# Kernel tuning notes

Hardware: AMD Instinct MI355X
Metric: run time of the kernel (lower is better)

Reference implementation:

```python
import jax, jax.numpy as jnp
import numpy as np

N = 32768   # 'a' nodes
K = 8       # incoming edges per node (regular graph)
K2 = K // 2
E = N * K   # edges, stored as reverse pairs (2i, 2i+1)
D = 300     # hid_dim
H = 4       # attention heads
DEPTH = 3


def _build_graph():
    i = np.arange(N)
    src = np.empty(E, np.int64)
    mail = np.empty((N, K), np.int64)
    for d in range(1, K2 + 1):
        base = 2 * (i * K2 + (d - 1))
        src[base] = i                 # edge i -> (i+d)%N
        src[base + 1] = (i + d) % N   # reverse edge (i+d)%N -> i
        # incoming edges of node v: ((v-d)->v) and ((v+d)->v)
        mail[:, 2 * (d - 1)] = 2 * (((i - d) % N) * K2 + (d - 1))
        mail[:, 2 * (d - 1) + 1] = 2 * (i * K2 + (d - 1)) + 1
    return src, mail


def setup_inputs() -> dict:
    key = jax.random.key(0)
    ks = jax.random.split(key, 12)
    s = 1.0 / np.sqrt(D)
    src, mail = _build_graph()
    return {
        'f': jax.random.normal(ks[0], (N, D), jnp.float32),
        'x': jax.random.normal(ks[1], (E, D), jnp.float32),
        'mail_idx': jnp.asarray(mail),
        'src_idx': jnp.asarray(src),
        'Wq': jax.random.normal(ks[2], (D, D), jnp.float32) * s,
        'bq': jnp.zeros((D,), jnp.float32),
        'Wk': jax.random.normal(ks[3], (D, D), jnp.float32) * s,
        'bk': jnp.zeros((D,), jnp.float32),
        'Wv': jax.random.normal(ks[4], (D, D), jnp.float32) * s,
        'bv': jnp.zeros((D,), jnp.float32),
        'Wo': jax.random.normal(ks[5], (D, D), jnp.float32) * s,
        'bo': jnp.zeros((D,), jnp.float32),
        'Wmp': jax.random.normal(ks[6], (DEPTH - 1, D, D), jnp.float32) * s,
        'bmp': jnp.zeros((DEPTH - 1, D), jnp.float32),
        'Wlast': jax.random.normal(ks[7], (3 * D, D), jnp.float32) * s,
        'blast': jnp.zeros((D,), jnp.float32),
    }


def _mha(q_in, k_in, v_in, Wq, bq, Wk, bk, Wv, bv, Wo, bo):
    # q_in: [N,1,D], k_in/v_in: [N,K,D]  (per-node neighborhood attention)
    dk = D // H
    q = (q_in @ Wq + bq).reshape(N, 1, H, dk).transpose(0, 2, 1, 3)
    k = (k_in @ Wk + bk).reshape(N, -1, H, dk).transpose(0, 2, 1, 3)
    v = (v_in @ Wv + bv).reshape(N, -1, H, dk).transpose(0, 2, 1, 3)
    scores = jnp.einsum('nhqd,nhkd->nhqk', q, k) / jnp.sqrt(jnp.float32(dk))
    p = jax.nn.softmax(scores, axis=-1)
    o = jnp.einsum('nhqk,nhkd->nhqd', p, v).transpose(0, 2, 1, 3).reshape(N, 1, D)
    return o @ Wo + bo


def reference(f, x, mail_idx, src_idx, Wq, bq, Wk, bk, Wv, bv, Wo, bo,
              Wmp, bmp, Wlast, blast):
    rev = jnp.arange(E) ^ 1  # reverse_edge: swap within consecutive pairs
    f_h = f              # init_node: f_h = f.clone()
    h = x                # init_edge: h = x.clone()
    for i in range(DEPTH - 1):
        mail = h[mail_idx]                    # copy_e mailbox [N,K,D]
        feat = f_h[:, None, :]                # [N,1,D]
        # add_attn: attn(feat, mail, mail + feat)
        f_h = _mha(feat, mail, mail + feat,
                   Wq, bq, Wk, bk, Wv, bv, Wo, bo)[:, 0, :]
        rev_h = h[rev]                        # paired reverse-edge feature
        m = f_h[src_idx] - rev_h              # del_reverse_message
        h = jax.nn.relu(x + m @ Wmp[i] + bmp[i])  # update_edge
    # final node update: Linear(cat([sum(mailbox h), f_h, f]))
    mail_sum = jnp.sum(h[mail_idx], axis=1)   # [N,D]
    f_final = jnp.concatenate([mail_sum, f_h, f], axis=1) @ Wlast + blast
    return f_final
```

## Files before the change

kernel.cpp:

```cpp
#include <hip/hip_runtime.h>

typedef unsigned short u16;
typedef unsigned int u32;
typedef __bf16 bf16x8 __attribute__((ext_vector_type(8)));
typedef float f32x4 __attribute__((ext_vector_type(4)));

#define N_NODES 32768
#define E_EDGES 262144
#define BQ_U16 26240
#define S75 0.11547005383792515f

__device__ __forceinline__ float b2f(u16 u) {
    union { u32 u; float f; } x; x.u = ((u32)u) << 16; return x.f;
}
__device__ __forceinline__ u16 f2b(float f) {
    union { float f; u32 u; } x; x.f = f;
    u32 r = x.u + 0x7FFF + ((x.u >> 16) & 1);
    return (u16)(r >> 16);
}

#define GLOAD16(g, l) \
    __builtin_amdgcn_global_load_lds((const __attribute__((address_space(1))) u32*)(g), \
                                     (__attribute__((address_space(3))) u32*)(l), 16, 0, 0)

__global__ void convT_k(const float* __restrict__ src, int R, int C,
                        u16* __restrict__ dst, int KP_, long total) {
    long id = (long)blockIdx.x * blockDim.x + threadIdx.x;
    if (id >= total) return;
    int n = (int)(id / KP_), k = (int)(id % KP_);
    dst[id] = (k < R && n < C) ? f2b(src[(long)k * C + n]) : (u16)0;
}

__global__ void convTq_k(const float* __restrict__ src, u16* __restrict__ dst) {
    int id = blockIdx.x * 256 + threadIdx.x;
    if (id >= 4 * BQ_U16) return;
    int q = id / BQ_U16, rem = id % BQ_U16;
    int r = rem / 328, c = rem % 328;
    int n = q * 80 + r;
    dst[id] = (c < 300 && n < 300) ? f2b(src[(long)c * 300 + n]) : (u16)0;
}

__global__ void wqkq_k(const float* __restrict__ Wq, const float* __restrict__ Wk,
                       u16* __restrict__ dst) {
    int id = blockIdx.x * 256 + threadIdx.x;
    if (id >= 16 * BQ_U16) return;
    int q = id / BQ_U16, rem = id % BQ_U16;
    int r = rem / 328, c = rem % 328;
    int h = q >> 2;
    int cc = (q & 3) * 80 + r;
    float acc = 0.f;
    if (c < 300 && cc < 300) {
        const float* wq = Wq + (long)c * 300 + 75 * h;
        const float* wk = Wk + (long)cc * 300 + 75 * h;
        for (int d = 0; d < 75; ++d) acc += wq[d] * wk[d];
        acc *= S75;
    }
    dst[id] = f2b(acc);
}

__global__ void bqk_k(const float* __restrict__ bq, const float* __restrict__ Wk,
                      float* __restrict__ dst) {
    int n = blockIdx.x * 256 + threadIdx.x;
    if (n >= 1280) return;
    int h = n / 320, cc = n % 320;
    float acc = 0.f;
    if (cc < 300) {
        const float* b = bq + 75 * h;
        const float* wk = Wk + (long)cc * 300 + 75 * h;
        for (int d = 0; d < 75; ++d) acc += b[d] * wk[d];
        acc *= S75;
    }
    dst[n] = acc;
}

__global__ void ucatp_k(const float* __restrict__ Wv, const float* __restrict__ Wo,
                        u16* __restrict__ dst) {
    long id = (long)blockIdx.x * 256 + threadIdx.x;
    if (id >= 4L * 5 * BQ_U16) return;
    int q = (int)(id / (5 * BQ_U16));
    int rem = (int)(id % (5 * BQ_U16));
    int ph = rem / BQ_U16;
    int rem2 = rem % BQ_U16;
    int r = rem2 / 328, c = rem2 % 328;
    int n = q * 80 + r;
    float acc = 0.f;
    if (n < 300 && c < 320) {
        if (ph < 4) {
            int a = c;
            if (a < 300) {
                const float* wv = Wv + (long)a * 300 + 75 * ph;
                const float* wo = Wo + (long)(75 * ph) * 300 + n;
                for (int d = 0; d < 75; ++d) acc += wv[d] * wo[(long)d * 300];
            }
        } else {
            int a = c;
            if (a < 300) {
                const float* wv = Wv + (long)a * 300;
                const float* wo = Wo + n;
                for (int d = 0; d < 300; ++d) acc += wv[d] * wo[(long)d * 300];
            }
        }
    }
    dst[id] = f2b(acc);
}

__global__ void bvo_k(const float* __restrict__ bv, const float* __restrict__ Wo,
                      const float* __restrict__ bo, float* __restrict__ dst) {
    int n = blockIdx.x * 256 + threadIdx.x;
    if (n >= 320) return;
    float acc = 0.f;
    if (n < 300) {
        for (int d = 0; d < 300; ++d) acc += bv[d] * Wo[(long)d * 300 + n];
        acc += bo[n];
    }
    dst[n] = acc;
}

__global__ void padconv_k(const float* __restrict__ src, int C,
                          u16* __restrict__ dst, int CP,
                          u16* __restrict__ dst2, int CP2, long total) {
    long id = (long)blockIdx.x * blockDim.x + threadIdx.x;
    if (id >= total) return;
    int cw = CP >> 3;
    long row = id / cw;
    int c8 = (int)(id % cw) * 8;
    u32 w[4];
    #pragma unroll
    for (int p = 0; p < 4; ++p) {
        int c0 = c8 + 2 * p, c1 = c0 + 1;
        u16 lo = (c0 < C) ? f2b(src[row * C + c0]) : (u16)0;
        u16 hi = (c1 < C) ? f2b(src[row * C + c1]) : (u16)0;
        w[p] = (u32)lo | ((u32)hi << 16);
    }
    u32* d = (u32*)(dst + row * CP + c8);
    d[0] = w[0]; d[1] = w[1]; d[2] = w[2]; d[3] = w[3];
    if (dst2) {
        u32* d2 = (u32*)(dst2 + row * CP2 + c8);
        d2[0] = w[0]; d2[1] = w[1]; d2[2] = w[2]; d2[3] = w[3];
    }
}

__global__ void featcopy_k(const u16* __restrict__ src, u16* __restrict__ dst) {
    long id = (long)blockIdx.x * 256 + threadIdx.x;
    if (id >= (long)N_NODES * 40) return;
    long row = id / 40;
    int c8 = (int)(id % 40) * 8;
    *(uint4*)&dst[row * 1600 + 1280 + c8] = *(const uint4*)&src[row * 320 + c8];
}

#define TCOMP(KB, APTR) do { \
    bf16x8 av_[2], bb_[5]; \
    _Pragma("unroll") for (int fr = 0; fr < 2; ++fr) \
        av_[fr] = *(const bf16x8*)&(APTR)[ar0 + fr * 512]; \
    _Pragma("unroll") for (int fc = 0; fc < 5; ++fc) \
        bb_[fc] = *(const bf16x8*)&Bs[br0 + fc * 5248 + (KB) * 32]; \
    __builtin_amdgcn_s_setprio(1); \
    _Pragma("unroll") for (int fr = 0; fr < 2; ++fr) \
        _Pragma("unroll") for (int fc = 0; fc < 5; ++fc) \
            acc[fr][fc] = __builtin_amdgcn_mfma_f32_16x16x32_bf16(bb_[fc], av_[fr], acc[fr][fc], 0, 0, 0); \
    __builtin_amdgcn_s_setprio(0); \
} while (0)

template<int QBITS, int OSTR>
__global__ __launch_bounds__(256, 2) void ngemm_k(
    const u16* __restrict__ A, const u16* __restrict__ Bswz,
    const float* __restrict__ bias, u16* __restrict__ outB)
{
    __shared__ __attribute__((aligned(16))) u16 Bs[80 * 328];
    __shared__ __attribute__((aligned(16))) u16 As3[3][128 * 32];
    const int tid = threadIdx.x;
    const int wf = tid >> 6, lane = tid & 63;
    const int tl = lane & 15, thi = lane >> 4;
    const int bid = blockIdx.x;
    const int gid = (bid & 7) * ((int)gridDim.x >> 3) + (bid >> 3);
    const long m0 = (long)(gid >> QBITS) * 128;
    const int q = gid & ((1 << QBITS) - 1);
    const int n0 = q * 80;
    const int wf_u = __builtin_amdgcn_readfirstlane(wf);
    const u16* Bsrc = Bswz + q * BQ_U16;

    #pragma unroll
    for (int i = 0; i < 13; ++i) {
        int t = i * 256 + tid;
        if (t < 3280)
            GLOAD16(Bsrc + (long)t * 8, &Bs[(i * 256 + wf_u * 64) * 8]);
    }
    const int r1 = tid >> 2;
    const int g1 = (tid & 3) ^ ((r1 >> 1) & 3);
    const u16* gA0 = A + (m0 + r1) * 320L + g1 * 8;
    const u16* gA1 = A + (m0 + 64 + r1) * 320L + g1 * 8;

#define ESTAGE(KB) { \
    GLOAD16(gA0 + (KB) * 32, &As3[(KB) % 3][wf_u * 512]); \
    GLOAD16(gA1 + (KB) * 32, &As3[(KB) % 3][2048 + wf_u * 512]); }

    ESTAGE(0); ESTAGE(1);

    f32x4 acc[2][5];
    #pragma unroll
    for (int i = 0; i < 2; ++i)
        #pragma unroll
        for (int j = 0; j < 5; ++j) acc[i][j] = (f32x4)(0.f);
    const int ar0 = (wf * 32 + tl) * 32 + (thi ^ ((tl >> 1) & 3)) * 8;
    const int br0 = tl * 328 + thi * 8;

#define ESTEP(KB, VN) { \
    asm volatile("s_waitcnt vmcnt(" #VN ")" ::: "memory"); \
    __builtin_amdgcn_s_barrier(); \
    __builtin_amdgcn_sched_barrier(0); \
    if ((KB) + 2 < 10) ESTAGE((KB) + 2); \
    TCOMP(KB, (&As3[(KB) % 3][0])); }

    ESTEP(0, 2) ESTEP(1, 2) ESTEP(2, 2) ESTEP(3, 2) ESTEP(4, 2)
    ESTEP(5, 2) ESTEP(6, 2) ESTEP(7, 2) ESTEP(8, 2) ESTEP(9, 0)
#undef ESTEP
#undef ESTAGE

    #pragma unroll
    for (int fr = 0; fr < 2; ++fr) {
        const long row = m0 + wf * 32 + fr * 16 + tl;
        #pragma unroll
        for (int fc = 0; fc < 5; ++fc) {
            const int c0 = n0 + fc * 16 + thi * 4;
            f32x4 v = acc[fr][fc];
            if (bias) {
                const float4 bs = *(const float4*)&bias[c0];
                v[0] += bs.x; v[1] += bs.y; v[2] += bs.z; v[3] += bs.w;
            }
            uint2 p;
            p.x = (u32)f2b(v[0]) | ((u32)f2b(v[1]) << 16);
            p.y = (u32)f2b(v[2]) | ((u32)f2b(v[3]) << 16);
            *(uint2*)&outB[row * (long)OSTR + c0] = p;
        }
    }
}

__global__ __launch_bounds__(256, 2) void hgemm_k(
    const u16* __restrict__ A , const u16* __restrict__ Bswz ,
    const u16* __restrict__ FG, const u16* __restrict__ hx,
    const int* __restrict__ srcidx, const float* __restrict__ bias,
    u16* __restrict__ outB)
{
    __shared__ __attribute__((aligned(16))) u16 Bs[80 * 328];
    __shared__ __attribute__((aligned(16))) u16 As3[3][128 * 32];
    const int tid = threadIdx.x;
    const int wf = tid >> 6, lane = tid & 63;
    const int tl = lane & 15, thi = lane >> 4;
    const int bid = blockIdx.x;
    const int gid = (bid & 7) * ((int)gridDim.x >> 3) + (bid >> 3);
    const long m0 = (long)(gid >> 2) * 128;
    const int q = gid & 3;
    const int n0 = q * 80;
    const int wf_u = __builtin_amdgcn_readfirstlane(wf);
    const u16* Bsrc = Bswz + q * BQ_U16;

    #pragma unroll
    for (int i = 0; i < 13; ++i) {
        int t = i * 256 + tid;
        if (t < 3280)
            GLOAD16(Bsrc + (long)t * 8, &Bs[(i * 256 + wf_u * 64) * 8]);
    }
    const int r1 = tid >> 2;
    const int g1 = (tid & 3) ^ ((r1 >> 1) & 3);
    const u16* gA0 = A + (m0 + r1) * 320L + g1 * 8;
    const u16* gA1 = A + (m0 + 64 + r1) * 320L + g1 * 8;

#define HSTAGE(KB) { \
    GLOAD16(gA0 + (KB) * 32, &As3[(KB) % 3][wf_u * 512]); \
    GLOAD16(gA1 + (KB) * 32, &As3[(KB) % 3][2048 + wf_u * 512]); }

    HSTAGE(0); HSTAGE(1);

    f32x4 acc[2][5];
    #pragma unroll
    for (int i = 0; i < 2; ++i)
        #pragma unroll
        for (int j = 0; j < 5; ++j) acc[i][j] = (f32x4)(0.f);
    const int ar0 = (wf * 32 + tl) * 32 + (thi ^ ((tl >> 1) & 3)) * 8;
    const int br0 = tl * 328 + thi * 8;

#define HSTEP(KB, VN) { \
    asm volatile("s_waitcnt vmcnt(" #VN ")" ::: "memory"); \
    __builtin_amdgcn_s_barrier(); \
    __builtin_amdgcn_sched_barrier(0); \
    if ((KB) + 2 < 10) HSTAGE((KB) + 2); \
    TCOMP(KB, (&As3[(KB) % 3][0])); }

    HSTEP(0, 2) HSTEP(1, 2) HSTEP(2, 2) HSTEP(3, 2) HSTEP(4, 2)
    HSTEP(5, 2) HSTEP(6, 2) HSTEP(7, 2) HSTEP(8, 2) HSTEP(9, 0)
#undef HSTEP
#undef HSTAGE

    #pragma unroll
    for (int fr = 0; fr < 2; ++fr) {
        const long row = m0 + wf * 32 + fr * 16 + tl;
        const int srow = srcidx[row];
        #pragma unroll
        for (int fc = 0; fc < 5; ++fc) {
            const int c0 = n0 + fc * 16 + thi * 4;
            float o0 = __shfl_xor(acc[fr][fc][0], 1, 64);
            float o1 = __shfl_xor(acc[fr][fc][1], 1, 64);
            float o2 = __shfl_xor(acc[fr][fc][2], 1, 64);
            float o3 = __shfl_xor(acc[fr][fc][3], 1, 64);
            const ushort4 fg = *(const ushort4*)&FG[(long)srow * 320 + c0];
            const ushort4 xv = *(const ushort4*)&hx[row * 320 + c0];
            float v0 = b2f(fg.x) + b2f(xv.x) - o0;
            float v1 = b2f(fg.y) + b2f(xv.y) - o1;
            float v2 = b2f(fg.z) + b2f(xv.z) - o2;
            float v3 = b2f(fg.w) + b2f(xv.w) - o3;
            if (c0 < 300) {
                const float4 bs = *(const float4*)&bias[c0];
                v0 += bs.x; v1 += bs.y; v2 += bs.z; v3 += bs.w;
            }
            v0 = fmaxf(v0, 0.f); v1 = fmaxf(v1, 0.f);
            v2 = fmaxf(v2, 0.f); v3 = fmaxf(v3, 0.f);
            uint2 p;
            p.x = (u32)f2b(v0) | ((u32)f2b(v1) << 16);
            p.y = (u32)f2b(v2) | ((u32)f2b(v3) << 16);
            *(uint2*)&outB[row * 320 + c0] = p;
        }
    }
}

__global__ __launch_bounds__(256, 2) void wgemm_k(
    const u16* __restrict__ A , const u16* __restrict__ Bp ,
    const float* __restrict__ bias , u16* __restrict__ outB )
{
    __shared__ __attribute__((aligned(16))) u16 Bs[80 * 328];
    __shared__ __attribute__((aligned(16))) u16 As3[3][128 * 32];
    const int tid = threadIdx.x;
    const int wf = tid >> 6, lane = tid & 63;
    const int tl = lane & 15, thi = lane >> 4;
    const int bid = blockIdx.x;
    const int gid = (bid & 7) * ((int)gridDim.x >> 3) + (bid >> 3);
    const long m0 = (long)(gid >> 2) * 128;
    const int q = gid & 3;
    const int n0 = q * 80;
    const int wf_u = __builtin_amdgcn_readfirstlane(wf);
    const u16* BsrcQ = Bp + (long)q * (5 * BQ_U16);

    const int r1 = tid >> 2;
    const int g1 = (tid & 3) ^ ((r1 >> 1) & 3);
    const u16* gA0 = A + (m0 + r1) * 1600L + g1 * 8;
    const u16* gA1 = A + (m0 + 64 + r1) * 1600L + g1 * 8;

    f32x4 acc[2][5];
    #pragma unroll
    for (int i = 0; i < 2; ++i)
        #pragma unroll
        for (int j = 0; j < 5; ++j) acc[i][j] = (f32x4)(0.f);
    const int ar0 = (wf * 32 + tl) * 32 + (thi ^ ((tl >> 1) & 3)) * 8;
    const int br0 = tl * 328 + thi * 8;

    #pragma unroll
    for (int ph = 0; ph < 5; ++ph) {
        if (ph) __syncthreads();
        const u16* Bsrc = BsrcQ + ph * BQ_U16;
        #pragma unroll
        for (int i = 0; i < 13; ++i) {
            int t = i * 256 + tid;
            if (t < 3280)
                GLOAD16(Bsrc + (long)t * 8, &Bs[(i * 256 + wf_u * 64) * 8]);
        }
        const long ko = (long)ph * 320;

#define WSTAGE(KB) { \
    GLOAD16(gA0 + ko + (KB) * 32, &As3[(KB) % 3][wf_u * 512]); \
    GLOAD16(gA1 + ko + (KB) * 32, &As3[(KB) % 3][2048 + wf_u * 512]); }

        WSTAGE(0); WSTAGE(1);

#define WSTEP(KB, VN) { \
    asm volatile("s_waitcnt vmcnt(" #VN ")" ::: "memory"); \
    __builtin_amdgcn_s_barrier(); \
    __builtin_amdgcn_sched_barrier(0); \
    if ((KB) + 2 < 10) WSTAGE((KB) + 2); \
    TCOMP(KB, (&As3[(KB) % 3][0])); }

        WSTEP(0, 2) WSTEP(1, 2) WSTEP(2, 2) WSTEP(3, 2) WSTEP(4, 2)
        WSTEP(5, 2) WSTEP(6, 2) WSTEP(7, 2) WSTEP(8, 2) WSTEP(9, 0)
#undef WSTEP
#undef WSTAGE
    }

    #pragma unroll
    for (int fr = 0; fr < 2; ++fr) {
        const long row = m0 + wf * 32 + fr * 16 + tl;
        #pragma unroll
        for (int fc = 0; fc < 5; ++fc) {
            const int c0 = n0 + fc * 16 + thi * 4;
            f32x4 v = acc[fr][fc];
            const float4 bs = *(const float4*)&bias[c0];
            v[0] += bs.x; v[1] += bs.y; v[2] += bs.z; v[3] += bs.w;
            uint2 p;
            p.x = (u32)f2b(v[0]) | ((u32)f2b(v[1]) << 16);
            p.y = (u32)f2b(v[2]) | ((u32)f2b(v[3]) << 16);
            *(uint2*)&outB[row * 320 + c0] = p;
        }
    }
}

__global__ __launch_bounds__(256) void attn2_k(
    const u16* __restrict__ qg, const u16* __restrict__ hcur,
    const int* __restrict__ mail, u16* __restrict__ wideA)
{
    const int tid = threadIdx.x;
    const long n = (long)blockIdx.x * 4 + (tid >> 6);
    const int lane = tid & 63;
    const bool act = lane < 40;
    const int ll = act ? lane : 39;

    int idx[8];
    #pragma unroll
    for (int j = 0; j < 8; ++j) idx[j] = mail[n * 8 + j];
    uint4 hr[8];
    #pragma unroll
    for (int j = 0; j < 8; ++j)
        hr[j] = *(const uint4*)&hcur[(long)idx[j] * 320 + ll * 8];
    uint4 qv[4];
    #pragma unroll
    for (int h = 0; h < 4; ++h)
        qv[h] = *(const uint4*)&qg[n * 1280 + h * 320 + ll * 8];
    if (!act) {
        #pragma unroll
        for (int j = 0; j < 8; ++j) hr[j] = make_uint4(0, 0, 0, 0);
    }

    float qf[4][8];
    #pragma unroll
    for (int h = 0; h < 4; ++h) {
        const u32 w[4] = {qv[h].x, qv[h].y, qv[h].z, qv[h].w};
        #pragma unroll
        for (int p = 0; p < 4; ++p) {
            qf[h][2 * p]     = b2f((u16)(w[p] & 0xFFFF));
            qf[h][2 * p + 1] = b2f((u16)(w[p] >> 16));
        }
    }

    float s[4][8];
    #pragma unroll
    for (int j = 0; j < 8; ++j) {
        float hf[8];
        const u32 w[4] = {hr[j].x, hr[j].y, hr[j].z, hr[j].w};
        #pragma unroll
        for (int p = 0; p < 4; ++p) {
            hf[2 * p]     = b2f((u16)(w[p] & 0xFFFF));
            hf[2 * p + 1] = b2f((u16)(w[p] >> 16));
        }
        #pragma unroll
        for (int h = 0; h < 4; ++h) {
            float d = 0.f;
            #pragma unroll
            for (int m = 0; m < 8; ++m) d += qf[h][m] * hf[m];
            d += __shfl_xor(d, 32, 64);
            d += __shfl_xor(d, 16, 64);
            d += __shfl_xor(d, 8, 64);
            d += __shfl_xor(d, 4, 64);
            d += __shfl_xor(d, 2, 64);
            d += __shfl_xor(d, 1, 64);
            s[h][j] = d;
        }
    }

    float p_[4][8];
    #pragma unroll
    for (int h = 0; h < 4; ++h) {
        float mx = s[h][0];
        #pragma unroll
        for (int j = 1; j < 8; ++j) mx = fmaxf(mx, s[h][j]);
        float sum = 0.f;
        #pragma unroll
        for (int j = 0; j < 8; ++j) { p_[h][j] = __expf(s[h][j] - mx); sum += p_[h][j]; }
        const float inv = 1.f / sum;
        #pragma unroll
        for (int j = 0; j < 8; ++j) p_[h][j] *= inv;
    }

    float y[4][8];
    #pragma unroll
    for (int h = 0; h < 4; ++h)
        #pragma unroll
        for (int m = 0; m < 8; ++m) y[h][m] = 0.f;
    #pragma unroll
    for (int j = 0; j < 8; ++j) {
        float hf[8];
        const u32 w[4] = {hr[j].x, hr[j].y, hr[j].z, hr[j].w};
        #pragma unroll
        for (int p = 0; p < 4; ++p) {
            hf[2 * p]     = b2f((u16)(w[p] & 0xFFFF));
            hf[2 * p + 1] = b2f((u16)(w[p] >> 16));
        }
        #pragma unroll
        for (int h = 0; h < 4; ++h)
            #pragma unroll
            for (int m = 0; m < 8; ++m) y[h][m] += p_[h][j] * hf[m];
    }
    if (act) {
        #pragma unroll
        for (int h = 0; h < 4; ++h) {
            uint4 o;
            o.x = (u32)f2b(y[h][0]) | ((u32)f2b(y[h][1]) << 16);
            o.y = (u32)f2b(y[h][2]) | ((u32)f2b(y[h][3]) << 16);
            o.z = (u32)f2b(y[h][4]) | ((u32)f2b(y[h][5]) << 16);
            o.w = (u32)f2b(y[h][6]) | ((u32)f2b(y[h][7]) << 16);
            *(uint4*)&wideA[n * 1600 + h * 320 + lane * 8] = o;
        }
    }
}

#define LOADB(bq, kt1) { const long ko_ = (long)(kt1) << 6; \
    _Pragma("unroll") for (int fc = 0; fc < 5; ++fc) \
      _Pragma("unroll") for (int ks = 0; ks < 2; ++ks) \
        bq[fc][ks] = *(const bf16x8*)(gBw + (long)fc * 16 * KP + ko_ + ks * 32); }

#define READA(lkt) { \
    _Pragma("unroll") for (int fr = 0; fr < 4; ++fr) \
      _Pragma("unroll") for (int ks = 0; ks < 2; ++ks) \
        a[fr][ks] = *(const bf16x8*)&As[(fr * 16 + tl) * 320 + ((((lkt) * 8 + ks * 4 + thi) ^ sx) * 8)]; }

#define DOMFMA(bq) { _Pragma("unroll") for (int fr = 0; fr < 4; ++fr) \
    _Pragma("unroll") for (int fc = 0; fc < 5; ++fc) \
      _Pragma("unroll") for (int ks = 0; ks < 2; ++ks) \
        acc[fr][fc] = __builtin_amdgcn_mfma_f32_16x16x32_bf16(bq[fc][ks], a[fr][ks], acc[fr][fc], 0, 0, 0); }

template<int KP>
__global__ __launch_bounds__(256, 2) void gemm_k(
    const u16* __restrict__ A,
    const u16* __restrict__ BT,
    const float* __restrict__ bias,
    float* __restrict__ outF, int ostride, int ocols)
{
    __shared__ u16 As[64 * 320];
    const int tid = threadIdx.x;
    const int w = tid >> 6, lane = tid & 63;
    const int tl = lane & 15, thi = lane >> 4;
    const int sx = tl & 7;
    const long m0 = (long)blockIdx.x * 64;
    const int w_u = __builtin_amdgcn_readfirstlane(w);

    const u16* gBw = BT + ((long)(w * 80 + tl)) * KP + thi * 8;

    f32x4 acc[4][5];
    #pragma unroll
    for (int i = 0; i < 4; ++i)
        #pragma unroll
        for (int j = 0; j < 5; ++j) acc[i][j] = (f32x4)(0.f);

    constexpr int NCH = KP / 320;
    constexpr int NST = KP >> 6;
    bf16x8 bA[5][2], bB[5][2], a[4][2];

    #pragma unroll
    for (int kb = 0; kb < NCH; ++kb) {
        if (kb) __syncthreads();
        #pragma unroll
        for (int i = 0; i < 10; ++i) {
            const int c = i * 256 + w_u * 64 + lane;
            const int r = c / 40, s = c - r * 40;
            GLOAD16(A + (m0 + r) * (long)KP + kb * 320 + ((s ^ (r & 7)) * 8),
                    &As[(i * 256 + w_u * 64) * 8]);
        }
        if (kb == 0) LOADB(bA, 0);
        __syncthreads();
        #pragma unroll
        for (int lkt = 0; lkt < 5; ++lkt) {
            const int kt = kb * 5 + lkt;
            if (kt + 1 < NST) {
                if (kt & 1) { LOADB(bA, kt + 1); } else { LOADB(bB, kt + 1); }
            }
            READA(lkt);
            if (kt & 1) { DOMFMA(bB); } else { DOMFMA(bA); }
        }
    }

    #pragma unroll
    for (int fr = 0; fr < 4; ++fr) {
        const long row = m0 + fr * 16 + tl;
        #pragma unroll
        for (int fc = 0; fc < 5; ++fc) {
            const int c0 = w * 80 + fc * 16 + thi * 4;
            f32x4 v = acc[fr][fc];
            if (bias && c0 < 300) {
                const float4 bs = *(const float4*)&bias[c0];
                v[0] += bs.x; v[1] += bs.y; v[2] += bs.z; v[3] += bs.w;
            }
            if (c0 < ocols)
                *(float4*)&outF[row * (long)ostride + c0] = make_float4(v[0], v[1], v[2], v[3]);
        }
    }
}

__global__ __launch_bounds__(256) void concat_k(
    const u16* __restrict__ hb, const u16* __restrict__ fhb,
    const float* __restrict__ f, const int* __restrict__ mail,
    u16* __restrict__ Acat)
{
    const long n = blockIdx.x;
    int m[8];
    #pragma unroll
    for (int j = 0; j < 8; ++j) m[j] = mail[n * 8 + j];
    for (int c = threadIdx.x; c < 960; c += 256) {
        float v;
        if (c < 300) {
            float s = 0.f;
            #pragma unroll
            for (int j = 0; j < 8; ++j) s += b2f(hb[(long)m[j] * 320 + c]);
            v = s;
        } else if (c < 600) v = b2f(fhb[n * 320 + (c - 300)]);
        else if (c < 900) v = f[n * 300 + (c - 600)];
        else v = 0.f;
        Acat[n * 960 + c] = f2b(v);
    }
}

extern "C" void kernel_launch(void* const* d_in, const int* in_sizes, int n_in,
                              void* d_out, int out_size, void* d_ws, size_t ws_size,
                              hipStream_t stream)
{
    const int N = N_NODES, E = E_EDGES;
    const float* f    = (const float*)d_in[0];
    const float* x    = (const float*)d_in[1];
    const int*   mail = (const int*)d_in[2];
    const int*   srcx = (const int*)d_in[3];
    const float* Wq = (const float*)d_in[4];   const float* bq = (const float*)d_in[5];
    const float* Wk = (const float*)d_in[6];
    const float* Wv = (const float*)d_in[8];   const float* bv = (const float*)d_in[9];
    const float* Wo = (const float*)d_in[10];  const float* bo = (const float*)d_in[11];
    const float* Wmp = (const float*)d_in[12]; const float* bmp = (const float*)d_in[13];
    const float* Wlast = (const float*)d_in[14]; const float* blast = (const float*)d_in[15];
    float* out = (float*)d_out;

    char* ws = (char*)d_ws;
    size_t off = 0;
    auto alloc = [&](size_t b) -> void* {
        void* p = ws + off; off += (b + 255) & ~(size_t)255; return p;
    };
    u16* hb    = (u16*)alloc((size_t)E * 320 * 2);
    u16* hb2   = (u16*)alloc((size_t)E * 320 * 2);
    u16* qgb   = (u16*)alloc((size_t)N * 1280 * 2);
    u16* wideA = (u16*)alloc((size_t)N * 1600 * 2);
    u16* fhb   = (u16*)alloc((size_t)N * 320 * 2);
    u16* FGb   = (u16*)alloc((size_t)N * 320 * 2);
    u16* Acat  = (u16*)alloc((size_t)N * 960 * 2);
    u16* WqkS  = (u16*)alloc((size_t)16 * BQ_U16 * 2);
    u16* Wm0S  = (u16*)alloc((size_t)4 * BQ_U16 * 2);
    u16* Wm1S  = (u16*)alloc((size_t)4 * BQ_U16 * 2);
    u16* UcatP = (u16*)alloc((size_t)4 * 5 * BQ_U16 * 2);
    u16* WcatB = (u16*)alloc((size_t)960 * 320 * 2);
    float* bqkF = (float*)alloc(1280 * 4);
    float* bvoF = (float*)alloc(320 * 4);

    {
        wqkq_k<<<(16 * BQ_U16 + 255) / 256, 256, 0, stream>>>(Wq, Wk, WqkS);
        bqk_k<<<5, 256, 0, stream>>>(bq, Wk, bqkF);
        ucatp_k<<<(int)((4L * 5 * BQ_U16 + 255) / 256), 256, 0, stream>>>(Wv, Wo, UcatP);
        bvo_k<<<2, 256, 0, stream>>>(bv, Wo, bo, bvoF);
        int blks = (4 * BQ_U16 + 255) / 256;
        convTq_k<<<blks, 256, 0, stream>>>(Wmp, Wm0S);
        convTq_k<<<blks, 256, 0, stream>>>(Wmp + 90000, Wm1S);
        long totc = (long)320 * 960;
        convT_k<<<(int)((totc + 255) / 256), 256, 0, stream>>>(Wlast, 900, 300, WcatB, 960, totc);
    }
    {
        long totE = (long)E * 40;
        padconv_k<<<(int)((totE + 255) / 256), 256, 0, stream>>>(x, 300, hb, 320, nullptr, 0, totE);
        long totN = (long)N * 40;
        padconv_k<<<(int)((totN + 255) / 256), 256, 0, stream>>>(f, 300, fhb, 320, wideA + 1280, 1600, totN);
    }

    const int GQG = (N / 128) * 16;
    const int GNQ = (N / 128) * 4;
    const int GEH = (E / 128) * 4;

    for (int it = 0; it < 2; ++it) {
        const float* bmpi = bmp + it * 300;
        const u16* WmS = it ? Wm1S : Wm0S;
        const u16* hcur = it ? hb2 : hb;
        u16* hnxt = it ? hb : hb2;
        ngemm_k<4, 1280><<<GQG, 256, 0, stream>>>(fhb, WqkS, bqkF, qgb);
        attn2_k<<<N / 4, 256, 0, stream>>>(qgb, hcur, mail, wideA);
        wgemm_k<<<GNQ, 256, 0, stream>>>(wideA, UcatP, bvoF, fhb);
        featcopy_k<<<(int)(((long)N * 40 + 255) / 256), 256, 0, stream>>>(fhb, wideA);
        ngemm_k<2, 320><<<GNQ, 256, 0, stream>>>(fhb, WmS, nullptr, FGb);
        hgemm_k<<<GEH, 256, 0, stream>>>(hcur, WmS, FGb, hb, srcx, bmpi, hnxt);
    }

    concat_k<<<N, 256, 0, stream>>>(hb, fhb, f, mail, Acat);
    gemm_k<960><<<N / 64, 256, 0, stream>>>(Acat, WcatB, blast, out, 300, 300);
}
```

Before: 1.395 ms.

## Use 1024-thread 512-row tiles for node and edge GEMMs to amortize B loads

The ngemm and hgemm kernels move from 256-thread blocks with 128-row M tiles to 1024-thread blocks with 512-row tiles. Each wavefront now owns its own 32-row A slab, staged three K-blocks deep. The shared 80-column B panel is loaded once per block, so its global traffic and LDS fill are spread over four times as many rows. Per-K-step block barriers are replaced by per-wave vmcnt/lgkmcnt waits, because each wave only reads A data it loaded itself. In exchange, grids get smaller, the block needs more LDS and must fit 16 waves, and a few lanes issue dummy B loads into a scratch buffer.

```diff
diff --git a/kernel.cpp b/kernel.cpp
--- a/kernel.cpp
+++ b/kernel.cpp
@@ -148,77 +148,91 @@
     *(uint4*)&dst[row * 1600 + 1280 + c8] = *(const uint4*)&src[row * 320 + c8];
 }
 
-#define TCOMP(KB, APTR) do { \
-    bf16x8 av_[2], bb_[5]; \
-    _Pragma("unroll") for (int fr = 0; fr < 2; ++fr) \
-        av_[fr] = *(const bf16x8*)&(APTR)[ar0 + fr * 512]; \
-    _Pragma("unroll") for (int fc = 0; fc < 5; ++fc) \
-        bb_[fc] = *(const bf16x8*)&Bs[br0 + fc * 5248 + (KB) * 32]; \
+
+#define GEMM16_SHARED \
+    __shared__ __attribute__((aligned(16))) u16 Bs[3328 * 8];      \
+    __shared__ __attribute__((aligned(16))) u16 dumpB[512];        \
+    __shared__ __attribute__((aligned(16))) u16 As3[3][512 * 32];
+
+#define GEMM16_PRE(QBITS, LDA) \
+    const int tid = threadIdx.x; \
+    const int w = tid >> 6, lane = tid & 63; \
+    const int tl = lane & 15, thi = lane >> 4; \
+    const int bid = blockIdx.x; \
+    const int gid = (bid & 7) * ((int)gridDim.x >> 3) + (bid >> 3); \
+    const long m0 = (long)(gid >> (QBITS)) * 512; \
+    const int q = gid & ((1 << (QBITS)) - 1); \
+    const int n0 = q * 80; \
+    const int w_u = __builtin_amdgcn_readfirstlane(w); \
+    const u16* Bsrc = Bswz + q * BQ_U16; \
+     \
+    _Pragma("unroll") \
+    for (int i = 0; i < 3; ++i) \
+        GLOAD16(Bsrc + (long)(i * 1024 + tid) * 8, &Bs[(i * 1024 + w_u * 64) * 8]); \
+    { \
+        int t = 3072 + tid; \
+        int ts = t < 3280 ? t : 3279; \
+        u16* bdst = (w_u < 4) ? &Bs[(3072 + w_u * 64) * 8] : dumpB; \
+        GLOAD16(Bsrc + (long)ts * 8, bdst); \
+    } \
+    __builtin_amdgcn_sched_barrier(0); \
+     \
+    const int rr = lane >> 2;                  \
+    const int gsrc = (lane & 3) ^ (rr & 3);    \
+    const u16* pA0 = A + (m0 + w * 32 + rr) * (long)(LDA) + gsrc * 8; \
+    const u16* pA1 = pA0 + 16L * (LDA); \
+    u16* awbase = &As3[0][0];
+
+#define ASTAGE16(KB) { \
+    u16* d_ = &As3[(KB) % 3][w_u * 1024]; \
+    GLOAD16(pA0 + (KB) * 32, d_); \
+    GLOAD16(pA1 + (KB) * 32, d_ + 512); }
+
+#define TCOMP16(KB) { \
+    const u16* aw_ = &As3[(KB) % 3][w * 1024]; \
+    bf16x8 a0_ = *(const bf16x8*)&aw_[tl * 32 + (thi ^ (tl & 3)) * 8]; \
+    bf16x8 a1_ = *(const bf16x8*)&aw_[512 + tl * 32 + (thi ^ (tl & 3)) * 8]; \
     __builtin_amdgcn_s_setprio(1); \
-    _Pragma("unroll") for (int fr = 0; fr < 2; ++fr) \
-        _Pragma("unroll") for (int fc = 0; fc < 5; ++fc) \
-            acc[fr][fc] = __builtin_amdgcn_mfma_f32_16x16x32_bf16(bb_[fc], av_[fr], acc[fr][fc], 0, 0, 0); \
-    __builtin_amdgcn_s_setprio(0); \
-} while (0)
+    _Pragma("unroll") for (int fc = 0; fc < 5; ++fc) { \
+        bf16x8 bb_ = *(const bf16x8*)&Bs[tl * 328 + thi * 8 + fc * 5248 + (KB) * 32]; \
+        acc[0][fc] = __builtin_amdgcn_mfma_f32_16x16x32_bf16(bb_, a0_, acc[0][fc], 0, 0, 0); \
+        acc[1][fc] = __builtin_amdgcn_mfma_f32_16x16x32_bf16(bb_, a1_, acc[1][fc], 0, 0, 0); } \
+    __builtin_amdgcn_s_setprio(0); }
+
+#define GEMM16_LOOP \
+    ASTAGE16(0); ASTAGE16(1); ASTAGE16(2); \
+    f32x4 acc[2][5]; \
+    _Pragma("unroll") for (int i = 0; i < 2; ++i) \
+        _Pragma("unroll") for (int j = 0; j < 5; ++j) acc[i][j] = (f32x4)(0.f); \
+    asm volatile("s_waitcnt vmcnt(6)" ::: "memory");    \
+    __builtin_amdgcn_s_barrier();                       \
+    __builtin_amdgcn_sched_barrier(0); \
+     \
+    _Pragma("unroll") \
+    for (int KB = 0; KB < 10; ++KB) { \
+        if (KB <= 7)      { asm volatile("s_waitcnt vmcnt(4)" ::: "memory"); } \
+        else if (KB == 8) { asm volatile("s_waitcnt vmcnt(2)" ::: "memory"); } \
+        else              { asm volatile("s_waitcnt vmcnt(0)" ::: "memory"); } \
+        __builtin_amdgcn_sched_barrier(0); \
+        TCOMP16(KB); \
+        asm volatile("s_waitcnt lgkmcnt(0)" ::: "memory");   \
+        __builtin_amdgcn_sched_barrier(0); \
+        if (KB + 3 < 10) ASTAGE16(KB + 3); \
+    } \
+    (void)awbase;
 
 template<int QBITS, int OSTR>
-__global__ __launch_bounds__(256, 2) void ngemm_k(
+__global__ __launch_bounds__(1024, 4) void ngemm16_k(
     const u16* __restrict__ A, const u16* __restrict__ Bswz,
     const float* __restrict__ bias, u16* __restrict__ outB)
 {
-    __shared__ __attribute__((aligned(16))) u16 Bs[80 * 328];
-    __shared__ __attribute__((aligned(16))) u16 As3[3][128 * 32];
-    const int tid = threadIdx.x;
-    const int wf = tid >> 6, lane = tid & 63;
-    const int tl = lane & 15, thi = lane >> 4;
-    const int bid = blockIdx.x;
-    const int gid = (bid & 7) * ((int)gridDim.x >> 3) + (bid >> 3);
-    const long m0 = (long)(gid >> QBITS) * 128;
-    const int q = gid & ((1 << QBITS) - 1);
-    const int n0 = q * 80;
-    const int wf_u = __builtin_amdgcn_readfirstlane(wf);
-    const u16* Bsrc = Bswz + q * BQ_U16;
-
-    #pragma unroll
-    for (int i = 0; i < 13; ++i) {
-        int t = i * 256 + tid;
-        if (t < 3280)
-            GLOAD16(Bsrc + (long)t * 8, &Bs[(i * 256 + wf_u * 64) * 8]);
-    }
-    const int r1 = tid >> 2;
-    const int g1 = (tid & 3) ^ ((r1 >> 1) & 3);
-    const u16* gA0 = A + (m0 + r1) * 320L + g1 * 8;
-    const u16* gA1 = A + (m0 + 64 + r1) * 320L + g1 * 8;
-
-#define ESTAGE(KB) { \
-    GLOAD16(gA0 + (KB) * 32, &As3[(KB) % 3][wf_u * 512]); \
-    GLOAD16(gA1 + (KB) * 32, &As3[(KB) % 3][2048 + wf_u * 512]); }
-
-    ESTAGE(0); ESTAGE(1);
-
-    f32x4 acc[2][5];
-    #pragma unroll
-    for (int i = 0; i < 2; ++i)
-        #pragma unroll
-        for (int j = 0; j < 5; ++j) acc[i][j] = (f32x4)(0.f);
-    const int ar0 = (wf * 32 + tl) * 32 + (thi ^ ((tl >> 1) & 3)) * 8;
-    const int br0 = tl * 328 + thi * 8;
-
-#define ESTEP(KB, VN) { \
-    asm volatile("s_waitcnt vmcnt(" #VN ")" ::: "memory"); \
-    __builtin_amdgcn_s_barrier(); \
-    __builtin_amdgcn_sched_barrier(0); \
-    if ((KB) + 2 < 10) ESTAGE((KB) + 2); \
-    TCOMP(KB, (&As3[(KB) % 3][0])); }
-
-    ESTEP(0, 2) ESTEP(1, 2) ESTEP(2, 2) ESTEP(3, 2) ESTEP(4, 2)
-    ESTEP(5, 2) ESTEP(6, 2) ESTEP(7, 2) ESTEP(8, 2) ESTEP(9, 0)
-#undef ESTEP
-#undef ESTAGE
+    GEMM16_SHARED
+    GEMM16_PRE(QBITS, 320)
+    GEMM16_LOOP
 
     #pragma unroll
     for (int fr = 0; fr < 2; ++fr) {
-        const long row = m0 + wf * 32 + fr * 16 + tl;
+        const long row = m0 + w * 32 + fr * 16 + tl;
         #pragma unroll
         for (int fc = 0; fc < 5; ++fc) {
             const int c0 = n0 + fc * 16 + thi * 4;
@@ -235,65 +249,19 @@
     }
 }
 
-__global__ __launch_bounds__(256, 2) void hgemm_k(
+__global__ __launch_bounds__(1024, 4) void hgemm16_k(
     const u16* __restrict__ A , const u16* __restrict__ Bswz ,
     const u16* __restrict__ FG, const u16* __restrict__ hx,
     const int* __restrict__ srcidx, const float* __restrict__ bias,
     u16* __restrict__ outB)
 {
-    __shared__ __attribute__((aligned(16))) u16 Bs[80 * 328];
-    __shared__ __attribute__((aligned(16))) u16 As3[3][128 * 32];
-    const int tid = threadIdx.x;
-    const int wf = tid >> 6, lane = tid & 63;
-    const int tl = lane & 15, thi = lane >> 4;
-    const int bid = blockIdx.x;
-    const int gid = (bid & 7) * ((int)gridDim.x >> 3) + (bid >> 3);
-    const long m0 = (long)(gid >> 2) * 128;
-    const int q = gid & 3;
-    const int n0 = q * 80;
-    const int wf_u = __builtin_amdgcn_readfirstlane(wf);
-    const u16* Bsrc = Bswz + q * BQ_U16;
-
-    #pragma unroll
-    for (int i = 0; i < 13; ++i) {
-        int t = i * 256 + tid;
-        if (t < 3280)
-            GLOAD16(Bsrc + (long)t * 8, &Bs[(i * 256 + wf_u * 64) * 8]);
-    }
-    const int r1 = tid >> 2;
-    const int g1 = (tid & 3) ^ ((r1 >> 1) & 3);
-    const u16* gA0 = A + (m0 + r1) * 320L + g1 * 8;
-    const u16* gA1 = A + (m0 + 64 + r1) * 320L + g1 * 8;
-
-#define HSTAGE(KB) { \
-    GLOAD16(gA0 + (KB) * 32, &As3[(KB) % 3][wf_u * 512]); \
-    GLOAD16(gA1 + (KB) * 32, &As3[(KB) % 3][2048 + wf_u * 512]); }
-
-    HSTAGE(0); HSTAGE(1);
-
-    f32x4 acc[2][5];
-    #pragma unroll
-    for (int i = 0; i < 2; ++i)
-        #pragma unroll
-        for (int j = 0; j < 5; ++j) acc[i][j] = (f32x4)(0.f);
-    const int ar0 = (wf * 32 + tl) * 32 + (thi ^ ((tl >> 1) & 3)) * 8;
-    const int br0 = tl * 328 + thi * 8;
-
-#define HSTEP(KB, VN) { \
-    asm volatile("s_waitcnt vmcnt(" #VN ")" ::: "memory"); \
-    __builtin_amdgcn_s_barrier(); \
-    __builtin_amdgcn_sched_barrier(0); \
-    if ((KB) + 2 < 10) HSTAGE((KB) + 2); \
-    TCOMP(KB, (&As3[(KB) % 3][0])); }
-
-    HSTEP(0, 2) HSTEP(1, 2) HSTEP(2, 2) HSTEP(3, 2) HSTEP(4, 2)
-    HSTEP(5, 2) HSTEP(6, 2) HSTEP(7, 2) HSTEP(8, 2) HSTEP(9, 0)
-#undef HSTEP
-#undef HSTAGE
+    GEMM16_SHARED
+    GEMM16_PRE(2, 320)
+    GEMM16_LOOP
 
     #pragma unroll
     for (int fr = 0; fr < 2; ++fr) {
-        const long row = m0 + wf * 32 + fr * 16 + tl;
+        const long row = m0 + w * 32 + fr * 16 + tl;
         const int srow = srcidx[row];
         #pragma unroll
         for (int fc = 0; fc < 5; ++fc) {
@@ -322,11 +290,24 @@
     }
 }
 
+#define TCOMP(KB, APTR) do { \
+    bf16x8 av_[2], bb_[5]; \
+    _Pragma("unroll") for (int fr = 0; fr < 2; ++fr) \
+        av_[fr] = *(const bf16x8*)&(APTR)[ar0 + fr * 512]; \
+    _Pragma("unroll") for (int fc = 0; fc < 5; ++fc) \
+        bb_[fc] = *(const bf16x8*)&Bsw[br0 + fc * 5248 + (KB) * 32]; \
+    __builtin_amdgcn_s_setprio(1); \
+    _Pragma("unroll") for (int fr = 0; fr < 2; ++fr) \
+        _Pragma("unroll") for (int fc = 0; fc < 5; ++fc) \
+            acc[fr][fc] = __builtin_amdgcn_mfma_f32_16x16x32_bf16(bb_[fc], av_[fr], acc[fr][fc], 0, 0, 0); \
+    __builtin_amdgcn_s_setprio(0); \
+} while (0)
+
 __global__ __launch_bounds__(256, 2) void wgemm_k(
-    const u16* __restrict__ A , const u16* __restrict__ Bp ,
-    const float* __restrict__ bias , u16* __restrict__ outB )
+    const u16* __restrict__ A , const u16* __restrict__ Bp,
+    const float* __restrict__ bias, u16* __restrict__ outB)
 {
-    __shared__ __attribute__((aligned(16))) u16 Bs[80 * 328];
+    __shared__ __attribute__((aligned(16))) u16 Bsw[80 * 328];
     __shared__ __attribute__((aligned(16))) u16 As3[3][128 * 32];
     const int tid = threadIdx.x;
     const int wf = tid >> 6, lane = tid & 63;
@@ -360,7 +341,7 @@
         for (int i = 0; i < 13; ++i) {
             int t = i * 256 + tid;
             if (t < 3280)
-                GLOAD16(Bsrc + (long)t * 8, &Bs[(i * 256 + wf_u * 64) * 8]);
+                GLOAD16(Bsrc + (long)t * 8, &Bsw[(i * 256 + wf_u * 64) * 8]);
         }
         const long ko = (long)ph * 320;
 
@@ -668,21 +649,22 @@
         padconv_k<<<(int)((totN + 255) / 256), 256, 0, stream>>>(f, 300, fhb, 320, wideA + 1280, 1600, totN);
     }
 
-    const int GQG = (N / 128) * 16;
-    const int GNQ = (N / 128) * 4;
-    const int GEH = (E / 128) * 4;
+    const int GQG = (N / 512) * 16;
+    const int GFG = (N / 512) * 4;
+    const int GNW = (N / 128) * 4;
+    const int GEH = (E / 512) * 4;
 
     for (int it = 0; it < 2; ++it) {
         const float* bmpi = bmp + it * 300;
         const u16* WmS = it ? Wm1S : Wm0S;
         const u16* hcur = it ? hb2 : hb;
         u16* hnxt = it ? hb : hb2;
-        ngemm_k<4, 1280><<<GQG, 256, 0, stream>>>(fhb, WqkS, bqkF, qgb);
+        ngemm16_k<4, 1280><<<GQG, 1024, 0, stream>>>(fhb, WqkS, bqkF, qgb);
         attn2_k<<<N / 4, 256, 0, stream>>>(qgb, hcur, mail, wideA);
-        wgemm_k<<<GNQ, 256, 0, stream>>>(wideA, UcatP, bvoF, fhb);
+        wgemm_k<<<GNW, 256, 0, stream>>>(wideA, UcatP, bvoF, fhb);
         featcopy_k<<<(int)(((long)N * 40 + 255) / 256), 256, 0, stream>>>(fhb, wideA);
-        ngemm_k<2, 320><<<GNQ, 256, 0, stream>>>(fhb, WmS, nullptr, FGb);
-        hgemm_k<<<GEH, 256, 0, stream>>>(hcur, WmS, FGb, hb, srcx, bmpi, hnxt);
+        ngemm16_k<2, 320><<<GFG, 1024, 0, stream>>>(fhb, WmS, nullptr, FGb);
+        hgemm16_k<<<GEH, 1024, 0, stream>>>(hcur, WmS, FGb, hb, srcx, bmpi, hnxt);
     }
 
     concat_k<<<N, 256, 0, stream>>>(hb, fhb, f, mail, Acat);
```

New measurement: 1.337 ms. -4.2%, faster.
